# Optimization experiments

Measured on AMD Instinct MI355X. Metric: run time of the kernel, lower is better.

## Reference

```python
import jax, jax.numpy as jnp
import numpy as np

B, L, D, H, T = 64, 512, 768, 384, 9  # batch, seq_len, hidden, hidden//2, num_tags


def setup_inputs() -> dict:
    key = jax.random.key(0)
    ks = jax.random.split(key, 8)
    return {
        "encoder_out": jax.random.normal(ks[0], (B, L, D), jnp.float32),
        "ner_labels": jax.random.randint(ks[1], (B, L), 0, T),
        "mask": jnp.ones((B, L), jnp.bool_),
        "W1": jax.random.normal(ks[2], (D, H), jnp.float32) / np.sqrt(D).astype(np.float32),
        "b1": jnp.zeros((H,), jnp.float32),
        "W2": jax.random.normal(ks[3], (H, T), jnp.float32) / np.sqrt(H).astype(np.float32),
        "b2": jnp.zeros((T,), jnp.float32),
        "start_trans": jax.random.uniform(ks[4], (T,), jnp.float32, -0.1, 0.1),
        "end_trans": jax.random.uniform(ks[5], (T,), jnp.float32, -0.1, 0.1),
        "trans": jax.random.uniform(ks[6], (T, T), jnp.float32, -0.1, 0.1),
    }


def _crf_nll(emissions, tags, mask, start_trans, end_trans, trans):
    """-mean log-likelihood, matching pytorch-crf forward (reduction='mean')."""
    maskf = mask.astype(emissions.dtype)
    # ---- numerator: score of the gold tag path ----
    emit = jnp.take_along_axis(emissions, tags[..., None], axis=-1)[..., 0]  # [B,L]
    emit_score = jnp.sum(emit * maskf, axis=1)
    tr = trans[tags[:, :-1], tags[:, 1:]]  # [B,L-1]
    tr_score = jnp.sum(tr * maskf[:, 1:], axis=1)
    last_idx = jnp.sum(mask.astype(jnp.int32), axis=1) - 1
    last_tags = jnp.take_along_axis(tags, last_idx[:, None], axis=1)[:, 0]
    numer = start_trans[tags[:, 0]] + emit_score + tr_score + end_trans[last_tags]
    # ---- denominator: forward algorithm (log partition) via scan ----
    alpha0 = start_trans[None, :] + emissions[:, 0]          # [B,T]
    em_rest = jnp.swapaxes(emissions[:, 1:], 0, 1)           # [L-1,B,T]
    mk_rest = jnp.swapaxes(maskf[:, 1:], 0, 1)               # [L-1,B]

    def step(alpha, xs):
        e_t, m_t = xs
        nxt = jax.nn.logsumexp(alpha[:, :, None] + trans[None, :, :] + e_t[:, None, :], axis=1)
        return jnp.where(m_t[:, None] > 0, nxt, alpha), None

    alpha, _ = jax.lax.scan(step, alpha0, (em_rest, mk_rest))
    denom = jax.nn.logsumexp(alpha + end_trans[None, :], axis=1)
    return -jnp.mean(numer - denom)


def reference(encoder_out, ner_labels, mask, W1, b1, W2, b2, start_trans, end_trans, trans):
    # proj: Linear -> GELU (exact erf, torch default) -> Dropout (identity in eval)
    h = jax.nn.gelu(encoder_out @ W1 + b1, approximate=False)
    emissions = h @ W2 + b2  # [B,L,T]
    return _crf_nll(emissions, ner_labels, mask, start_trans, end_trans, trans)
```

## Files before the change

kernel.cpp:

```cpp
#include <hip/hip_runtime.h>
#include <hip/hip_bf16.h>
#include <math.h>

#define B_ 64
#define L_ 512
#define D_ 768
#define H_ 384
#define T_ 9
#define M_ (B_ * L_)

typedef __attribute__((ext_vector_type(8))) short short8;
typedef __attribute__((ext_vector_type(4))) float f32x4;

__device__ __forceinline__ unsigned short f2bf(float f) {
    unsigned u = __float_as_uint(f);
    u += 0x7FFFu + ((u >> 16) & 1u);
    return (unsigned short)(u >> 16);
}

__device__ __forceinline__ unsigned pkbf2(float a, float b) {
    __hip_bfloat162 h = __float22bfloat162_rn(float2{a, b});
    return *(unsigned*)&h;
}

__device__ __forceinline__ float gelu_fast(float x) {
    float z2 = 1.5957691216f * x + 0.0713548162726f * x * x * x;
    return x / (1.f + __expf(-z2));
}

__device__ __forceinline__ float wredf(float v) {
#pragma unroll
    for (int m = 32; m >= 1; m >>= 1) v += __shfl_xor(v, m, 64);
    return v;
}

__device__ __forceinline__ void sync_lds() {
    asm volatile("s_waitcnt lgkmcnt(0)\n\ts_barrier" ::: "memory");
}

__global__ __launch_bounds__(256) void prep_kernel(
    const float* __restrict__ W1, const float* __restrict__ W2,
    unsigned short* __restrict__ W1F, unsigned short* __restrict__ W2F,
    float* __restrict__ out)
{
    if (blockIdx.x == 0 && threadIdx.x == 0) out[0] = 0.f;
    const int g    = blockIdx.x * 4 + (threadIdx.x >> 6);
    const int lane = threadIdx.x & 63;
    const int lm   = lane & 15;
    const int q    = lane >> 4;
    if (g < 576) {
        const int nt = g / 24;
        const int kc = g - nt * 24;
        const int n  = nt * 16 + lm;
        short8 v;
#pragma unroll
        for (int j = 0; j < 8; ++j)
            v[j] = (short)f2bf(W1[(size_t)(kc * 32 + q * 8 + j) * H_ + n]);
        *(short8*)(W1F + ((size_t)g * 64 + lane) * 8) = v;
    } else if (g < 588) {
        const int kk = g - 576;
        short8 v;
#pragma unroll
        for (int j = 0; j < 8; ++j) {
            int k = kk * 32 + q * 8 + j;
            v[j] = (lm < 9) ? (short)f2bf(W2[(size_t)k * T_ + lm]) : (short)0;
        }
        *(short8*)(W2F + ((size_t)kk * 64 + lane) * 8) = v;
    }
}

__global__ __launch_bounds__(256, 4) void emis_mfma_kernel(
    const float* __restrict__ X,
    const unsigned short* __restrict__ W1F,
    const float* __restrict__ b1,
    const unsigned short* __restrict__ W2F,
    const float* __restrict__ b2,
    float* __restrict__ em)
{
    __shared__ unsigned short Hs[32 * 392];
    unsigned short* As = Hs;

    const int t    = threadIdx.x;
    const int lane = t & 63;
    const int w    = t >> 6;
    const int lm   = lane & 15;
    const int q    = lane >> 4;
    const int row0 = blockIdx.x * 32;

    const int sr = t >> 3;
    const int sk = (t & 7) << 2;
    const float* xp = X + (size_t)(row0 + sr) * D_ + sk;

    f32x4 acc[2][6];
#pragma unroll
    for (int mt = 0; mt < 2; ++mt)
#pragma unroll
        for (int i = 0; i < 6; ++i) acc[mt][i] = (f32x4)0.f;

    {
        float4 x0 = *(const float4*)xp;
        int2 v = {(int)pkbf2(x0.x, x0.y), (int)pkbf2(x0.z, x0.w)};
        *(int2*)&As[sr * 40 + sk] = v;
    }

#pragma unroll
    for (int kc = 0; kc < 24; ++kc) {
        const int s = kc & 1;
        float4 xn;
        if (kc < 23) xn = *(const float4*)(xp + (kc + 1) * 32);
        sync_lds();
        short8 af[2];
#pragma unroll
        for (int mt = 0; mt < 2; ++mt)
            af[mt] = *(const short8*)&As[s * 1280 + (mt * 16 + lm) * 40 + (q << 3)];
#pragma unroll
        for (int i = 0; i < 6; ++i) {
            short8 bf = *(const short8*)(W1F +
                (((size_t)(w * 6 + i) * 24 + kc) * 64 + lane) * 8);
            acc[0][i] = __builtin_amdgcn_mfma_f32_16x16x32_bf16(af[0], bf, acc[0][i], 0, 0, 0);
            acc[1][i] = __builtin_amdgcn_mfma_f32_16x16x32_bf16(af[1], bf, acc[1][i], 0, 0, 0);
        }
        if (kc < 23) {
            int2 v = {(int)pkbf2(xn.x, xn.y), (int)pkbf2(xn.z, xn.w)};
            *(int2*)&As[(s ^ 1) * 1280 + sr * 40 + sk] = v;
        }
    }
    __syncthreads();

#pragma unroll
    for (int i = 0; i < 6; ++i) {
        const int col = w * 96 + i * 16 + lm;
        const float b1v = b1[col];
#pragma unroll
        for (int mt = 0; mt < 2; ++mt)
#pragma unroll
            for (int r = 0; r < 4; ++r) {
                float h = gelu_fast(acc[mt][i][r] + b1v);
                Hs[(mt * 16 + q * 4 + r) * 392 + col] = f2bf(h);
            }
    }
    __syncthreads();

    if (w < 2) {
        f32x4 e = (f32x4)0.f;
#pragma unroll
        for (int kk = 0; kk < 12; ++kk) {
            short8 ah = *(const short8*)&Hs[(w * 16 + lm) * 392 + kk * 32 + (q << 3)];
            short8 bw = *(const short8*)(W2F + ((size_t)(kk * 64 + lane)) * 8);
            e = __builtin_amdgcn_mfma_f32_16x16x32_bf16(ah, bw, e, 0, 0, 0);
        }
        if (lm < 9) {
            const float b2v = b2[lm];
#pragma unroll
            for (int r = 0; r < 4; ++r)
                em[(size_t)(row0 + w * 16 + q * 4 + r) * T_ + lm] = e[r] + b2v;
        }
    }
}

__global__ __launch_bounds__(576) void crf_kernel(
    const float* __restrict__ em,
    const int* __restrict__ labels,
    const unsigned char* __restrict__ maskb,
    const float* __restrict__ st,
    const float* __restrict__ et,
    const float* __restrict__ tr,
    float* __restrict__ out)
{
    const int b = blockIdx.x;
    const int t = threadIdx.x;

    __shared__ float es[64 * 73];
    __shared__ float Ms[64 * 81];
    __shared__ float trs[81];
    __shared__ float red[2];
    __shared__ unsigned char msh[L_];
    __shared__ int lbs[L_];

    const int mstride =
        (maskb[0] != 0 && maskb[1] == 0 && maskb[2] == 0 && maskb[3] == 0) ? 4 : 1;

    const float* eb = em + (size_t)b * L_ * T_;
    for (int i = t; i < L_ * T_; i += 576) {
        int tt = i / T_, j = i - tt * T_;
        es[(tt >> 3) * 73 + (tt & 7) * 9 + j] = eb[i];
    }
    if (t < 81) trs[t] = tr[t];
    for (int i = t; i < L_; i += 576) {
        msh[i] = maskb[((size_t)b * L_ + i) * (size_t)mstride];
        lbs[i] = labels[b * L_ + i];
    }
    __syncthreads();

    {
        const int c  = t / 9;
        const int i0 = t - c * 9;
        float trr[81];
#pragma unroll
        for (int i = 0; i < 81; ++i) trr[i] = trs[i];
        float V[9];
#pragma unroll
        for (int j = 0; j < 9; ++j) V[j] = (j == i0) ? 0.f : -1e30f;

        const int sbeg = (c == 0) ? 1 : 0;
        for (int s = sbeg; s < 8; ++s) {
            int tt = c * 8 + s;
            if (msh[tt]) {
                const float* ep = &es[c * 73 + s * 9];
                float nv[9];
#pragma unroll
                for (int j = 0; j < 9; ++j) {
                    float a[9];
#pragma unroll
                    for (int k = 0; k < 9; ++k) a[k] = V[k] + trr[k * 9 + j];
                    float mx = a[0];
#pragma unroll
                    for (int k = 1; k < 9; ++k) mx = fmaxf(mx, a[k]);
                    float sum = 0.f;
#pragma unroll
                    for (int k = 0; k < 9; ++k) sum += __expf(a[k] - mx);
                    nv[j] = ep[j] + mx + __logf(sum);
                }
#pragma unroll
                for (int j = 0; j < 9; ++j) V[j] = nv[j];
            }
        }
#pragma unroll
        for (int j = 0; j < 9; ++j) Ms[c * 81 + i0 * 9 + j] = V[j];
    }
    __syncthreads();

    const int lane = t & 63;
    const int w    = t >> 6;
    if (w == 0) {
        const int jj = lane < 9 ? lane : 8;
        float alpha = (lane < 9) ? st[jj] + es[jj] : -1e30f;
        for (int c = 0; c < 64; ++c) {
            float a[9];
#pragma unroll
            for (int i = 0; i < 9; ++i) {
                float av = __shfl(alpha, i, 64);
                a[i] = av + Ms[c * 81 + i * 9 + jj];
            }
            float mx = a[0];
#pragma unroll
            for (int i = 1; i < 9; ++i) mx = fmaxf(mx, a[i]);
            float sum = 0.f;
#pragma unroll
            for (int i = 0; i < 9; ++i) sum += __expf(a[i] - mx);
            float nv = mx + __logf(sum);
            if (lane < 9) alpha = nv;
        }
        float v = (lane < 9) ? alpha + et[jj] : -1e30f;
        float mx = v;
#pragma unroll
        for (int m = 32; m >= 1; m >>= 1) mx = fmaxf(mx, __shfl_xor(mx, m, 64));
        float s = __expf(v - mx);
        s = wredf(s);
        if (lane == 0) red[0] = mx + __logf(s);
    } else if (w == 1) {
        float emit_s = 0.f, tr_sc = 0.f, mcnt = 0.f;
        for (int tt = lane; tt < L_; tt += 64) {
            if (msh[tt]) {
                mcnt += 1.f;
                int tag = lbs[tt];
                emit_s += es[(tt >> 3) * 73 + (tt & 7) * 9 + tag];
                if (tt >= 1) tr_sc += trs[lbs[tt - 1] * 9 + tag];
            }
        }
        emit_s = wredf(emit_s);
        tr_sc  = wredf(tr_sc);
        mcnt   = wredf(mcnt);
        if (lane == 0) {
            int last = (int)mcnt - 1;
            red[1] = st[lbs[0]] + emit_s + tr_sc + et[lbs[last]];
        }
    }
    __syncthreads();
    if (t == 0) atomicAdd(out, (red[0] - red[1]) * (1.0f / (float)B_));
}

extern "C" void kernel_launch(void* const* d_in, const int* in_sizes, int n_in,
                              void* d_out, int out_size, void* d_ws, size_t ws_size,
                              hipStream_t stream) {
    const float*         enc    = (const float*)d_in[0];
    const int*           labels = (const int*)d_in[1];
    const unsigned char* mask   = (const unsigned char*)d_in[2];
    const float*         W1     = (const float*)d_in[3];
    const float*         b1     = (const float*)d_in[4];
    const float*         W2     = (const float*)d_in[5];
    const float*         b2     = (const float*)d_in[6];
    const float*         st     = (const float*)d_in[7];
    const float*         et     = (const float*)d_in[8];
    const float*         tr     = (const float*)d_in[9];

    float* em           = (float*)d_ws;
    unsigned short* W1F = (unsigned short*)(em + (size_t)M_ * T_);
    unsigned short* W2F = W1F + (size_t)576 * 64 * 8;

    prep_kernel<<<147, 256, 0, stream>>>(W1, W2, W1F, W2F, (float*)d_out);
    emis_mfma_kernel<<<M_ / 32, 256, 0, stream>>>(enc, W1F, b1, W2F, b2, em);
    crf_kernel<<<B_, 576, 0, stream>>>(em, labels, mask, st, et, tr, (float*)d_out);
}
```

Measured before the change: 239.7 us.

## Double GEMM row tile to 64 and load A fragments directly from global

The emission kernel now handles 64 rows per block instead of 32, with each wave holding 4x6 MFMA accumulators, so every W1 fragment is reused across twice as many rows. The LDS double-buffered staging of X and its per-iteration barriers are removed; each lane loads its bf16 A fragment straight from global memory and converts it in registers. All four waves now take part in the second small GEMM. The cost is higher register pressure (launch bounds lowered to 2 blocks per SM), half as many blocks, and no software prefetch of X, so global latency may be less hidden.

```diff
diff --git a/kernel.cpp b/kernel.cpp
--- a/kernel.cpp
+++ b/kernel.cpp
@@ -32,10 +32,6 @@
 #pragma unroll
     for (int m = 32; m >= 1; m >>= 1) v += __shfl_xor(v, m, 64);
     return v;
-}
-
-__device__ __forceinline__ void sync_lds() {
-    asm volatile("s_waitcnt lgkmcnt(0)\n\ts_barrier" ::: "memory");
 }
 
 __global__ __launch_bounds__(256) void prep_kernel(
@@ -69,7 +65,7 @@
     }
 }
 
-__global__ __launch_bounds__(256, 4) void emis_mfma_kernel(
+__global__ __launch_bounds__(256, 2) void emis_mfma_kernel(
     const float* __restrict__ X,
     const unsigned short* __restrict__ W1F,
     const float* __restrict__ b1,
@@ -77,62 +73,60 @@
     const float* __restrict__ b2,
     float* __restrict__ em)
 {
-    __shared__ unsigned short Hs[32 * 392];
-    unsigned short* As = Hs;
+    __shared__ unsigned short Hs[64 * 392];
 
     const int t    = threadIdx.x;
     const int lane = t & 63;
     const int w    = t >> 6;
     const int lm   = lane & 15;
     const int q    = lane >> 4;
-    const int row0 = blockIdx.x * 32;
-
-    const int sr = t >> 3;
-    const int sk = (t & 7) << 2;
-    const float* xp = X + (size_t)(row0 + sr) * D_ + sk;
-
-    f32x4 acc[2][6];
-#pragma unroll
-    for (int mt = 0; mt < 2; ++mt)
+    const int row0 = blockIdx.x * 64;
+
+    const float* xa[4];
+#pragma unroll
+    for (int mt = 0; mt < 4; ++mt)
+        xa[mt] = X + (size_t)(row0 + mt * 16 + lm) * D_ + (q << 3);
+
+    const unsigned short* bp[6];
+#pragma unroll
+    for (int i = 0; i < 6; ++i)
+        bp[i] = W1F + ((size_t)(w * 6 + i) * 24 * 64 + lane) * 8;
+
+    f32x4 acc[4][6];
+#pragma unroll
+    for (int mt = 0; mt < 4; ++mt)
 #pragma unroll
         for (int i = 0; i < 6; ++i) acc[mt][i] = (f32x4)0.f;
 
-    {
-        float4 x0 = *(const float4*)xp;
-        int2 v = {(int)pkbf2(x0.x, x0.y), (int)pkbf2(x0.z, x0.w)};
-        *(int2*)&As[sr * 40 + sk] = v;
-    }
-
 #pragma unroll
     for (int kc = 0; kc < 24; ++kc) {
-        const int s = kc & 1;
-        float4 xn;
-        if (kc < 23) xn = *(const float4*)(xp + (kc + 1) * 32);
-        sync_lds();
-        short8 af[2];
-#pragma unroll
-        for (int mt = 0; mt < 2; ++mt)
-            af[mt] = *(const short8*)&As[s * 1280 + (mt * 16 + lm) * 40 + (q << 3)];
-#pragma unroll
-        for (int i = 0; i < 6; ++i) {
-            short8 bf = *(const short8*)(W1F +
-                (((size_t)(w * 6 + i) * 24 + kc) * 64 + lane) * 8);
-            acc[0][i] = __builtin_amdgcn_mfma_f32_16x16x32_bf16(af[0], bf, acc[0][i], 0, 0, 0);
-            acc[1][i] = __builtin_amdgcn_mfma_f32_16x16x32_bf16(af[1], bf, acc[1][i], 0, 0, 0);
-        }
-        if (kc < 23) {
-            int2 v = {(int)pkbf2(xn.x, xn.y), (int)pkbf2(xn.z, xn.w)};
-            *(int2*)&As[(s ^ 1) * 1280 + sr * 40 + sk] = v;
-        }
-    }
-    __syncthreads();
+        short8 af[4];
+#pragma unroll
+        for (int mt = 0; mt < 4; ++mt) {
+            float4 a0 = *(const float4*)(xa[mt] + kc * 32);
+            float4 a1 = *(const float4*)(xa[mt] + kc * 32 + 4);
+            int4 iv = {(int)pkbf2(a0.x, a0.y), (int)pkbf2(a0.z, a0.w),
+                       (int)pkbf2(a1.x, a1.y), (int)pkbf2(a1.z, a1.w)};
+            af[mt] = *(short8*)&iv;
+        }
+        short8 bf[6];
+#pragma unroll
+        for (int i = 0; i < 6; ++i)
+            bf[i] = *(const short8*)(bp[i] + (size_t)kc * 512);
+#pragma unroll
+        for (int mt = 0; mt < 4; ++mt)
+#pragma unroll
+            for (int i = 0; i < 6; ++i)
+                acc[mt][i] = __builtin_amdgcn_mfma_f32_16x16x32_bf16(
+                    af[mt], bf[i], acc[mt][i], 0, 0, 0);
+    }
 
 #pragma unroll
     for (int i = 0; i < 6; ++i) {
         const int col = w * 96 + i * 16 + lm;
         const float b1v = b1[col];
 #pragma unroll
-        for (int mt = 0; mt < 2; ++mt)
+        for (int mt = 0; mt < 4; ++mt)
 #pragma unroll
             for (int r = 0; r < 4; ++r) {
                 float h = gelu_fast(acc[mt][i][r] + b1v);
@@ -141,20 +135,18 @@
     }
     __syncthreads();
 
-    if (w < 2) {
-        f32x4 e = (f32x4)0.f;
-#pragma unroll
-        for (int kk = 0; kk < 12; ++kk) {
-            short8 ah = *(const short8*)&Hs[(w * 16 + lm) * 392 + kk * 32 + (q << 3)];
-            short8 bw = *(const short8*)(W2F + ((size_t)(kk * 64 + lane)) * 8);
-            e = __builtin_amdgcn_mfma_f32_16x16x32_bf16(ah, bw, e, 0, 0, 0);
-        }
-        if (lm < 9) {
-            const float b2v = b2[lm];
-#pragma unroll
-            for (int r = 0; r < 4; ++r)
-                em[(size_t)(row0 + w * 16 + q * 4 + r) * T_ + lm] = e[r] + b2v;
-        }
+    f32x4 e = (f32x4)0.f;
+#pragma unroll
+    for (int kk = 0; kk < 12; ++kk) {
+        short8 ah = *(const short8*)&Hs[(w * 16 + lm) * 392 + kk * 32 + (q << 3)];
+        short8 bw = *(const short8*)(W2F + ((size_t)(kk * 64 + lane)) * 8);
+        e = __builtin_amdgcn_mfma_f32_16x16x32_bf16(ah, bw, e, 0, 0, 0);
+    }
+    if (lm < 9) {
+        const float b2v = b2[lm];
+#pragma unroll
+        for (int r = 0; r < 4; ++r)
+            em[(size_t)(row0 + w * 16 + q * 4 + r) * T_ + lm] = e[r] + b2v;
     }
 }
 
@@ -299,6 +291,6 @@
     unsigned short* W2F = W1F + (size_t)576 * 64 * 8;
 
     prep_kernel<<<147, 256, 0, stream>>>(W1, W2, W1F, W2F, (float*)d_out);
-    emis_mfma_kernel<<<M_ / 32, 256, 0, stream>>>(enc, W1F, b1, W2F, b2, em);
+    emis_mfma_kernel<<<M_ / 64, 256, 0, stream>>>(enc, W1F, b1, W2F, b2, em);
     crf_kernel<<<B_, 576, 0, stream>>>(em, labels, mask, st, et, tr, (float*)d_out);
 }
```

New measurement: 262.1 us. +9.4%, slower.
